# Kernel tuning notes

Hardware: AMD Instinct MI355X
Metric: run time of the kernel (lower is better)

## Reference

```python
import jax, jax.numpy as jnp
import numpy as np

N = 32768   # num nodes
E = 65536   # num edges
H = 64      # hidden_size
EH = 64     # edge_hidden_size
LN_EPS = 1e-5


def setup_inputs() -> dict:
    key = jax.random.key(0)
    ks = jax.random.split(key, 6)
    node_emb = jax.random.normal(ks[0], (N, H), dtype=jnp.float32)
    edge_emb = jax.random.normal(ks[1], (E, EH), dtype=jnp.float32)
    edge_index = jax.random.randint(ks[2], (2, E), 0, N, dtype=jnp.int64)
    # edge_weight_net MLP: edge_hidden -> hidden (relu) -> H*H, xavier-uniform style scales
    W1 = jax.random.normal(ks[3], (EH, H), dtype=jnp.float32) * (2.0 / (EH + H)) ** 0.5
    b1 = jnp.zeros((H,), dtype=jnp.float32)
    W2 = jax.random.normal(ks[4], (H, H * H), dtype=jnp.float32) * (2.0 / (H + H * H)) ** 0.5
    b2 = jnp.zeros((H * H,), dtype=jnp.float32)
    root = jax.random.normal(ks[5], (H, H), dtype=jnp.float32) * (2.0 / (H + H)) ** 0.5
    bias = jnp.zeros((H,), dtype=jnp.float32)
    gamma = jnp.ones((H,), dtype=jnp.float32)
    beta = jnp.zeros((H,), dtype=jnp.float32)
    return {"node_emb": node_emb, "edge_emb": edge_emb, "W1": W1, "b1": b1,
            "W2": W2, "b2": b2, "root": root, "bias": bias,
            "gamma": gamma, "beta": beta, "edge_index": edge_index}


def reference(node_emb, edge_emb, W1, b1, W2, b2, root, bias, gamma, beta, edge_index):
    src, dst = edge_index[0], edge_index[1]
    num_nodes = node_emb.shape[0]
    # edge-conditioned weight: MLP(edge_emb) -> per-edge [H, H] matrix ('full' mode)
    h = jax.nn.relu(edge_emb @ W1 + b1)                 # [E, H]
    W = (h @ W2 + b2).reshape(-1, H, H)                 # [E, H, H]
    # message = x_src @ W_e  (bmm of [1,H] x [H,H] per edge)
    msg = jnp.einsum('eh,ehk->ek', node_emb[src], W)    # [E, H]
    # scatter-add aggregation at destination nodes
    agg = jax.ops.segment_sum(msg, dst, num_segments=num_nodes)          # [N, H]
    deg = jax.ops.segment_sum(jnp.ones_like(dst, dtype=node_emb.dtype), dst,
                              num_segments=num_nodes)                    # [N]
    agg = agg / jnp.maximum(deg, 1.0)[:, None]          # 'mean' aggregation
    # root transform + bias + residual
    out = agg + node_emb @ root + bias + node_emb       # [N, H]
    # LayerNorm over hidden dim
    mu = jnp.mean(out, axis=-1, keepdims=True)
    var = jnp.var(out, axis=-1, keepdims=True)
    out = (out - mu) * jax.lax.rsqrt(var + LN_EPS) * gamma + beta
    return out
```

## Files before the change

### kernel.cpp

```cpp
#include <hip/hip_runtime.h>

#define N_NODES 32768
#define N_EDGES 65536

typedef _Float16 f16;
typedef _Float16 f16x8 __attribute__((ext_vector_type(8)));
typedef float f32x16 __attribute__((ext_vector_type(16)));

#define WS_AGG   0
#define WS_DEG   8388608
#define WS_W2    8519680
#define WS_W1    9060352
#define WS_ROOT  9068544

#define MFMA(a, b, c) __builtin_amdgcn_mfma_f32_32x32x16_f16((a), (b), (c), 0, 0, 0)

__device__ inline f16 u16_as_f16(unsigned short u) {
  union { unsigned short s; f16 h; } v; v.s = u; return v.h;
}
__device__ inline f16x8 splat8(f16 x) {
  f16x8 r;
  #pragma unroll
  for (int u = 0; u < 8; ++u) r[u] = x;
  return r;
}
__device__ inline f16x8 cvt8(float4 p0, float4 p1) {
  f16x8 a;
  a[0] = (f16)p0.x; a[1] = (f16)p0.y; a[2] = (f16)p0.z; a[3] = (f16)p0.w;
  a[4] = (f16)p1.x; a[5] = (f16)p1.y; a[6] = (f16)p1.z; a[7] = (f16)p1.w;
  return a;
}

__global__ __launch_bounds__(256) void k_prep(const float* __restrict__ W1,
                                              const float* __restrict__ W2,
                                              const float* __restrict__ b2,
                                              const float* __restrict__ root,
                                              const int* __restrict__ eidx,
                                              float* __restrict__ deg,
                                              char* __restrict__ w2v2,
                                              char* __restrict__ w1v2,
                                              char* __restrict__ rootIv2) {
  int t = blockIdx.x * 256 + threadIdx.x;
  if (t < 270336) {
    int oct = t >> 9, q = t & 511;
    int col = q >> 3, hl = q & 7;
    int j = oct >> 3, sub = oct & 7;
    int h = (sub >> 1) * 16 + (sub & 1) * 8 + hl;
    float v = 0.f;
    if (j < 64)       v = W2[j * 4096 + h * 64 + col];
    else if (j == 64) v = b2[h * 64 + col];
    *(f16*)(w2v2 + t * 2) = (f16)v;
  } else if (t < 274432) {
    int u = t - 270336;
    int oct = u >> 9, q = u & 511, col = q >> 3, hl = q & 7;
    int i = (oct >> 1) * 16 + (oct & 1) * 8 + hl;
    *(f16*)(w1v2 + u * 2) = (f16)W1[i * 64 + col];
  } else if (t < 278528) {
    int u = t - 274432;
    int oct = u >> 9, q = u & 511, col = q >> 3, hl = q & 7;
    int i = (oct >> 1) * 16 + (oct & 1) * 8 + hl;
    float v = root[i * 64 + col] + (i == col ? 1.f : 0.f);
    *(f16*)(rootIv2 + u * 2) = (f16)v;
  } else if (t < 344064) {
    int e = t - 278528;
    unsafeAtomicAdd(&deg[eidx[N_EDGES + e]], 1.0f);
  }
}

__global__ __launch_bounds__(256, 1) void k_main(const float* __restrict__ node,
                                                 const float* __restrict__ edge,
                                                 const float* __restrict__ b1,
                                                 const int* __restrict__ eidx,
                                                 const char* __restrict__ w2v2,
                                                 const char* __restrict__ w1v2,
                                                 float* __restrict__ agg) {
  __shared__ char ldsH[34816];

  const int tid = threadIdx.x;
  const int lane = tid & 63;
  const int wv = tid >> 6;
  const int ln31 = lane & 31;
  const int half = lane >> 5;
  const int ebase = blockIdx.x * 256;

  const char* w1p = w1v2 + half * 1024 + ln31 * 16;
  #pragma unroll
  for (int t = 0; t < 2; ++t) {
    const int tile = 2 * wv + t;
    const int e = ebase + tile * 32 + ln31;
    const float4* er = (const float4*)edge + (long)e * 16;
    f32x16 c0 = {}, c1 = {};
    #pragma unroll
    for (int kk = 0; kk < 4; ++kk) {
      f16x8 a = cvt8(er[kk * 4 + half * 2], er[kk * 4 + half * 2 + 1]);
      f16x8 bf0 = *(const f16x8*)(w1p + (kk * 2 << 10));
      f16x8 bf1 = *(const f16x8*)(w1p + (kk * 2 << 10) + 512);
      c0 = MFMA(a, bf0, c0);
      c1 = MFMA(a, bf1, c1);
    }
    const float bb0 = b1[ln31], bb1 = b1[32 + ln31];
    char* hb = ldsH + tile * 32 * 136;
    #pragma unroll
    for (int r = 0; r < 16; ++r) {
      const int m = (r & 3) + 8 * (r >> 2) + 4 * half;
      *(f16*)(hb + m * 136 + ln31 * 2)      = (f16)fmaxf(c0[r] + bb0, 0.f);
      *(f16*)(hb + m * 136 + 64 + ln31 * 2) = (f16)fmaxf(c1[r] + bb1, 0.f);
    }
  }

  const int ch = wv & 1;
  const int g  = wv >> 1;

  f16x8 xf[4][4];
  #pragma unroll
  for (int t = 0; t < 4; ++t) {
    const int e = ebase + (g * 4 + t) * 32 + ln31;
    const int s = eidx[e];
    const float4* xr = (const float4*)node + (long)s * 16;
    #pragma unroll
    for (int kk = 0; kk < 4; ++kk)
      xf[t][kk] = cvt8(xr[kk * 4 + half * 2], xr[kk * 4 + half * 2 + 1]);
  }

  const char* wp = w2v2 + half * 1024 + ch * 512 + ln31 * 16;
  f16x8 bufA[8], bufB[8];
  #pragma unroll
  for (int jj = 0; jj < 2; ++jj)
    #pragma unroll
    for (int kk = 0; kk < 4; ++kk)
      bufA[jj * 4 + kk] = *(const f16x8*)(wp + ((jj * 8 + kk * 2) << 10));

  f32x16 acc[4] = {};
  const char* hp[4];
  #pragma unroll
  for (int t = 0; t < 4; ++t) hp[t] = ldsH + (g * 128 + t * 32 + ln31) * 136;

  __syncthreads();

  for (int cp = 0; cp < 16; ++cp) {
    const char* base = wp + (cp << 15);
    uint2 hv[4];
    #pragma unroll
    for (int t = 0; t < 4; ++t) hv[t] = *(const uint2*)(hp[t] + cp * 8);

    #pragma unroll
    for (int jj = 0; jj < 2; ++jj)
      #pragma unroll
      for (int kk = 0; kk < 4; ++kk)
        bufB[jj * 4 + kk] = *(const f16x8*)(base + 16384 + ((jj * 8 + kk * 2) << 10));

    #pragma unroll
    for (int jj = 0; jj < 2; ++jj) {
      f16x8 sp[4];
      #pragma unroll
      for (int t = 0; t < 4; ++t)
        sp[t] = splat8(u16_as_f16((unsigned short)(hv[t].x >> (jj * 16))));
      #pragma unroll
      for (int kk = 0; kk < 4; ++kk)
        #pragma unroll
        for (int t = 0; t < 4; ++t)
          acc[t] = MFMA(xf[t][kk] * sp[t], bufA[jj * 4 + kk], acc[t]);
    }

    #pragma unroll
    for (int jj = 0; jj < 2; ++jj)
      #pragma unroll
      for (int kk = 0; kk < 4; ++kk)
        bufA[jj * 4 + kk] = *(const f16x8*)(base + 32768 + ((jj * 8 + kk * 2) << 10));

    #pragma unroll
    for (int jj = 0; jj < 2; ++jj) {
      f16x8 sp[4];
      #pragma unroll
      for (int t = 0; t < 4; ++t)
        sp[t] = splat8(u16_as_f16((unsigned short)(hv[t].y >> (jj * 16))));
      #pragma unroll
      for (int kk = 0; kk < 4; ++kk)
        #pragma unroll
        for (int t = 0; t < 4; ++t)
          acc[t] = MFMA(xf[t][kk] * sp[t], bufB[jj * 4 + kk], acc[t]);
    }
  }

  #pragma unroll
  for (int kk = 0; kk < 4; ++kk)
    #pragma unroll
    for (int t = 0; t < 4; ++t)
      acc[t] = MFMA(xf[t][kk], bufA[kk], acc[t]);

  #pragma unroll
  for (int t = 0; t < 4; ++t) {
    const int base_e = ebase + (g * 4 + t) * 32;
    #pragma unroll
    for (int r = 0; r < 16; ++r) {
      const int m = (r & 3) + 8 * (r >> 2) + 4 * half;
      const int d = eidx[N_EDGES + base_e + m];
      unsafeAtomicAdd(&agg[(long)d * 64 + ch * 32 + ln31], acc[t][r]);
    }
  }
}

__global__ __launch_bounds__(256) void k_node(const float* __restrict__ node,
                                              const float* __restrict__ agg,
                                              const float* __restrict__ deg,
                                              const char* __restrict__ rootIv2,
                                              const float* __restrict__ bias,
                                              const float* __restrict__ gamma,
                                              const float* __restrict__ beta,
                                              float* __restrict__ out) {
  const int tid = threadIdx.x;
  const int lane = tid & 63;
  const int wv = tid >> 6;
  const int ln31 = lane & 31;
  const int half = lane >> 5;
  const int nb = blockIdx.x * 128 + wv * 32;

  const char* rp = rootIv2 + half * 1024 + ln31 * 16;
  f32x16 c0 = {}, c1 = {};
  const float4* xr = (const float4*)node + (long)(nb + ln31) * 16;
  #pragma unroll
  for (int kk = 0; kk < 4; ++kk) {
    f16x8 a = cvt8(xr[kk * 4 + half * 2], xr[kk * 4 + half * 2 + 1]);
    f16x8 b0 = *(const f16x8*)(rp + (kk * 2 << 10));
    f16x8 b1f = *(const f16x8*)(rp + (kk * 2 << 10) + 512);
    c0 = MFMA(a, b0, c0);
    c1 = MFMA(a, b1f, c1);
  }
  const float bi0 = bias[ln31],  bi1 = bias[32 + ln31];
  const float g0  = gamma[ln31], g1  = gamma[32 + ln31];
  const float be0 = beta[ln31],  be1 = beta[32 + ln31];
  #pragma unroll
  for (int r = 0; r < 16; ++r) {
    const int m = (r & 3) + 8 * (r >> 2) + 4 * half;
    const int n = nb + m;
    const float rd = 1.f / fmaxf(deg[n], 1.f);
    const float pre0 = agg[n * 64 + ln31] * rd + c0[r] + bi0;
    const float pre1 = agg[n * 64 + 32 + ln31] * rd + c1[r] + bi1;
    float s = pre0 + pre1, s2 = pre0 * pre0 + pre1 * pre1;
    #pragma unroll
    for (int mk = 16; mk >= 1; mk >>= 1) {
      s  += __shfl_xor(s, mk, 64);
      s2 += __shfl_xor(s2, mk, 64);
    }
    const float mu  = s * 0.015625f;
    const float var = s2 * 0.015625f - mu * mu;
    const float inv = rsqrtf(var + 1e-5f);
    out[n * 64 + ln31]      = (pre0 - mu) * inv * g0 + be0;
    out[n * 64 + 32 + ln31] = (pre1 - mu) * inv * g1 + be1;
  }
}

extern "C" void kernel_launch(void* const* d_in, const int* in_sizes, int n_in,
                              void* d_out, int out_size, void* d_ws, size_t ws_size,
                              hipStream_t stream) {
  const float* node  = (const float*)d_in[0];
  const float* edgee = (const float*)d_in[1];
  const float* W1    = (const float*)d_in[2];
  const float* b1    = (const float*)d_in[3];
  const float* W2    = (const float*)d_in[4];
  const float* b2    = (const float*)d_in[5];
  const float* root  = (const float*)d_in[6];
  const float* bias  = (const float*)d_in[7];
  const float* gamma = (const float*)d_in[8];
  const float* beta  = (const float*)d_in[9];
  const int*   eidx  = (const int*)d_in[10];
  float* out = (float*)d_out;

  char* ws = (char*)d_ws;
  float* agg     = (float*)(ws + WS_AGG);
  float* deg     = (float*)(ws + WS_DEG);
  char*  w2v2    = ws + WS_W2;
  char*  w1v2    = ws + WS_W1;
  char*  rootIv2 = ws + WS_ROOT;

  hipMemsetAsync(ws, 0, 8519680, stream);

  k_prep<<<1344, 256, 0, stream>>>(W1, W2, b2, root, eidx, deg, w2v2, w1v2, rootIv2);
  k_main<<<256, 256, 0, stream>>>(node, edgee, b1, eidx, w2v2, w1v2, agg);
  k_node<<<256, 256, 0, stream>>>(node, agg, deg, rootIv2, bias, gamma, beta, out);
}
```

Before: 143.4 us.

## Double k_main wavefronts, halve per-wave edge tiles, and vectorize weight prep

k_main now runs 512 threads per block, so each wave handles two edge tiles instead of four. This cuts register pressure and raises the number of resident waves. The main loop is rewritten as a double-buffered chunk load/compute pipeline with s_setprio hints around the MFMA blocks. The b2 bias term is folded in by writing a constant 1.0 into the LDS hidden row. k_prep is also vectorized to read float4 and scatter f16 values, which cuts its thread count. The tradeoff is that each W2 fragment is reused across fewer edges per wave, so W2 traffic from L2 rises.

```diff
diff --git a/kernel.cpp b/kernel.cpp
--- a/kernel.cpp
+++ b/kernel.cpp
@@ -6,6 +6,7 @@
 typedef _Float16 f16;
 typedef _Float16 f16x8 __attribute__((ext_vector_type(8)));
 typedef float f32x16 __attribute__((ext_vector_type(16)));
+typedef unsigned int uint32;
 
 #define WS_AGG   0
 #define WS_DEG   8388608
@@ -41,33 +42,77 @@
                                               char* __restrict__ w1v2,
                                               char* __restrict__ rootIv2) {
   int t = blockIdx.x * 256 + threadIdx.x;
-  if (t < 270336) {
-    int oct = t >> 9, q = t & 511;
-    int col = q >> 3, hl = q & 7;
-    int j = oct >> 3, sub = oct & 7;
-    int h = (sub >> 1) * 16 + (sub & 1) * 8 + hl;
-    float v = 0.f;
-    if (j < 64)       v = W2[j * 4096 + h * 64 + col];
-    else if (j == 64) v = b2[h * 64 + col];
-    *(f16*)(w2v2 + t * 2) = (f16)v;
-  } else if (t < 274432) {
-    int u = t - 270336;
-    int oct = u >> 9, q = u & 511, col = q >> 3, hl = q & 7;
-    int i = (oct >> 1) * 16 + (oct & 1) * 8 + hl;
-    *(f16*)(w1v2 + u * 2) = (f16)W1[i * 64 + col];
-  } else if (t < 278528) {
-    int u = t - 274432;
-    int oct = u >> 9, q = u & 511, col = q >> 3, hl = q & 7;
-    int i = (oct >> 1) * 16 + (oct & 1) * 8 + hl;
-    float v = root[i * 64 + col] + (i == col ? 1.f : 0.f);
-    *(f16*)(rootIv2 + u * 2) = (f16)v;
-  } else if (t < 344064) {
-    int e = t - 278528;
+  if (t < 65536) {
+    int j = t >> 10, rem = t & 1023, h = rem >> 4, c4 = rem & 15;
+    float4 v = *(const float4*)(W2 + j * 4096 + h * 64 + c4 * 4);
+    int oct = j * 8 + (h >> 4) * 2 + ((h >> 3) & 1);
+    char* base = w2v2 + oct * 1024 + (h & 7) * 2;
+    *(f16*)(base + (c4 * 4 + 0) * 16) = (f16)v.x;
+    *(f16*)(base + (c4 * 4 + 1) * 16) = (f16)v.y;
+    *(f16*)(base + (c4 * 4 + 2) * 16) = (f16)v.z;
+    *(f16*)(base + (c4 * 4 + 3) * 16) = (f16)v.w;
+  } else if (t < 66560) {
+    int u = t - 65536, h = u >> 4, c4 = u & 15;
+    float4 v = *(const float4*)(b2 + h * 64 + c4 * 4);
+    int oct = 512 + (h >> 4) * 2 + ((h >> 3) & 1);
+    char* base = w2v2 + oct * 1024 + (h & 7) * 2;
+    *(f16*)(base + (c4 * 4 + 0) * 16) = (f16)v.x;
+    *(f16*)(base + (c4 * 4 + 1) * 16) = (f16)v.y;
+    *(f16*)(base + (c4 * 4 + 2) * 16) = (f16)v.z;
+    *(f16*)(base + (c4 * 4 + 3) * 16) = (f16)v.w;
+  } else if (t < 67584) {
+    int u = t - 66560, h = u >> 4, c4 = u & 15;
+    int oct = 520 + (h >> 4) * 2 + ((h >> 3) & 1);
+    char* base = w2v2 + oct * 1024 + (h & 7) * 2;
+    #pragma unroll
+    for (int q = 0; q < 4; ++q) *(f16*)(base + (c4 * 4 + q) * 16) = (f16)0.f;
+  } else if (t < 68608) {
+    int u = t - 67584, i = u >> 4, c4 = u & 15;
+    float4 v = *(const float4*)(W1 + i * 64 + c4 * 4);
+    int oct = (i >> 4) * 2 + ((i >> 3) & 1);
+    char* base = w1v2 + oct * 1024 + (i & 7) * 2;
+    *(f16*)(base + (c4 * 4 + 0) * 16) = (f16)v.x;
+    *(f16*)(base + (c4 * 4 + 1) * 16) = (f16)v.y;
+    *(f16*)(base + (c4 * 4 + 2) * 16) = (f16)v.z;
+    *(f16*)(base + (c4 * 4 + 3) * 16) = (f16)v.w;
+  } else if (t < 69632) {
+    int u = t - 68608, i = u >> 4, c4 = u & 15;
+    float4 v = *(const float4*)(root + i * 64 + c4 * 4);
+    int oct = (i >> 4) * 2 + ((i >> 3) & 1);
+    char* base = rootIv2 + oct * 1024 + (i & 7) * 2;
+    *(f16*)(base + (c4 * 4 + 0) * 16) = (f16)(v.x + (i == c4 * 4 + 0 ? 1.f : 0.f));
+    *(f16*)(base + (c4 * 4 + 1) * 16) = (f16)(v.y + (i == c4 * 4 + 1 ? 1.f : 0.f));
+    *(f16*)(base + (c4 * 4 + 2) * 16) = (f16)(v.z + (i == c4 * 4 + 2 ? 1.f : 0.f));
+    *(f16*)(base + (c4 * 4 + 3) * 16) = (f16)(v.w + (i == c4 * 4 + 3 ? 1.f : 0.f));
+  } else if (t < 135168) {
+    int e = t - 69632;
     unsafeAtomicAdd(&deg[eidx[N_EDGES + e]], 1.0f);
   }
 }
 
-__global__ __launch_bounds__(256, 1) void k_main(const float* __restrict__ node,
+__device__ inline void chunk_load(f16x8 (&buf)[8], const char* wp, int c) {
+  #pragma unroll
+  for (int jj = 0; jj < 2; ++jj)
+    #pragma unroll
+    for (int kk = 0; kk < 4; ++kk)
+      buf[jj * 4 + kk] = *(const f16x8*)(wp + c * 16384 + ((jj * 8 + kk * 2) << 10));
+}
+
+__device__ inline void chunk_compute(const f16x8 (&buf)[8], uint32 hA, uint32 hB,
+                                     const f16x8 (&xf)[2][4], f32x16 (&acc)[2]) {
+  #pragma unroll
+  for (int jj = 0; jj < 2; ++jj) {
+    const f16x8 spA = splat8(u16_as_f16((unsigned short)(hA >> (jj * 16))));
+    const f16x8 spB = splat8(u16_as_f16((unsigned short)(hB >> (jj * 16))));
+    #pragma unroll
+    for (int kk = 0; kk < 4; ++kk) {
+      acc[0] = MFMA(xf[0][kk] * spA, buf[jj * 4 + kk], acc[0]);
+      acc[1] = MFMA(xf[1][kk] * spB, buf[jj * 4 + kk], acc[1]);
+    }
+  }
+}
+
+__global__ __launch_bounds__(512, 2) void k_main(const float* __restrict__ node,
                                                  const float* __restrict__ edge,
                                                  const float* __restrict__ b1,
                                                  const int* __restrict__ eidx,
@@ -83,11 +128,9 @@
   const int half = lane >> 5;
   const int ebase = blockIdx.x * 256;
 
-  const char* w1p = w1v2 + half * 1024 + ln31 * 16;
-  #pragma unroll
-  for (int t = 0; t < 2; ++t) {
-    const int tile = 2 * wv + t;
-    const int e = ebase + tile * 32 + ln31;
+  {
+    const char* w1p = w1v2 + half * 1024 + ln31 * 16;
+    const int e = ebase + wv * 32 + ln31;
     const float4* er = (const float4*)edge + (long)e * 16;
     f32x16 c0 = {}, c1 = {};
     #pragma unroll
@@ -99,22 +142,24 @@
       c1 = MFMA(a, bf1, c1);
     }
     const float bb0 = b1[ln31], bb1 = b1[32 + ln31];
-    char* hb = ldsH + tile * 32 * 136;
+    char* hb = ldsH + wv * 32 * 136;
     #pragma unroll
     for (int r = 0; r < 16; ++r) {
       const int m = (r & 3) + 8 * (r >> 2) + 4 * half;
       *(f16*)(hb + m * 136 + ln31 * 2)      = (f16)fmaxf(c0[r] + bb0, 0.f);
       *(f16*)(hb + m * 136 + 64 + ln31 * 2) = (f16)fmaxf(c1[r] + bb1, 0.f);
     }
-  }
-
+    if (half == 0)
+      *(uint32*)(hb + ln31 * 136 + 128) = 0x00003C00u;
+  }
+
+  const int g = wv >> 1;
   const int ch = wv & 1;
-  const int g  = wv >> 1;
-
-  f16x8 xf[4][4];
-  #pragma unroll
-  for (int t = 0; t < 4; ++t) {
-    const int e = ebase + (g * 4 + t) * 32 + ln31;
+
+  f16x8 xf[2][4];
+  #pragma unroll
+  for (int t = 0; t < 2; ++t) {
+    const int e = ebase + (2 * g + t) * 32 + ln31;
     const int s = eidx[e];
     const float4* xr = (const float4*)node + (long)s * 16;
     #pragma unroll
@@ -123,74 +168,38 @@
   }
 
   const char* wp = w2v2 + half * 1024 + ch * 512 + ln31 * 16;
-  f16x8 bufA[8], bufB[8];
-  #pragma unroll
-  for (int jj = 0; jj < 2; ++jj)
-    #pragma unroll
-    for (int kk = 0; kk < 4; ++kk)
-      bufA[jj * 4 + kk] = *(const f16x8*)(wp + ((jj * 8 + kk * 2) << 10));
-
-  f32x16 acc[4] = {};
-  const char* hp[4];
-  #pragma unroll
-  for (int t = 0; t < 4; ++t) hp[t] = ldsH + (g * 128 + t * 32 + ln31) * 136;
+  const char* hpA = ldsH + ((2 * g + 0) * 32 + ln31) * 136;
+  const char* hpB = ldsH + ((2 * g + 1) * 32 + ln31) * 136;
+
+  f16x8 b0[8], b1v[8];
+  f32x16 acc[2] = {};
+  chunk_load(b0, wp, 0);
 
   __syncthreads();
 
-  for (int cp = 0; cp < 16; ++cp) {
-    const char* base = wp + (cp << 15);
-    uint2 hv[4];
-    #pragma unroll
-    for (int t = 0; t < 4; ++t) hv[t] = *(const uint2*)(hp[t] + cp * 8);
-
-    #pragma unroll
-    for (int jj = 0; jj < 2; ++jj)
-      #pragma unroll
-      for (int kk = 0; kk < 4; ++kk)
-        bufB[jj * 4 + kk] = *(const f16x8*)(base + 16384 + ((jj * 8 + kk * 2) << 10));
-
-    #pragma unroll
-    for (int jj = 0; jj < 2; ++jj) {
-      f16x8 sp[4];
-      #pragma unroll
-      for (int t = 0; t < 4; ++t)
-        sp[t] = splat8(u16_as_f16((unsigned short)(hv[t].x >> (jj * 16))));
-      #pragma unroll
-      for (int kk = 0; kk < 4; ++kk)
-        #pragma unroll
-        for (int t = 0; t < 4; ++t)
-          acc[t] = MFMA(xf[t][kk] * sp[t], bufA[jj * 4 + kk], acc[t]);
-    }
-
-    #pragma unroll
-    for (int jj = 0; jj < 2; ++jj)
-      #pragma unroll
-      for (int kk = 0; kk < 4; ++kk)
-        bufA[jj * 4 + kk] = *(const f16x8*)(base + 32768 + ((jj * 8 + kk * 2) << 10));
-
-    #pragma unroll
-    for (int jj = 0; jj < 2; ++jj) {
-      f16x8 sp[4];
-      #pragma unroll
-      for (int t = 0; t < 4; ++t)
-        sp[t] = splat8(u16_as_f16((unsigned short)(hv[t].y >> (jj * 16))));
-      #pragma unroll
-      for (int kk = 0; kk < 4; ++kk)
-        #pragma unroll
-        for (int t = 0; t < 4; ++t)
-          acc[t] = MFMA(xf[t][kk] * sp[t], bufB[jj * 4 + kk], acc[t]);
-    }
-  }
-
-  #pragma unroll
-  for (int kk = 0; kk < 4; ++kk)
-    #pragma unroll
-    for (int t = 0; t < 4; ++t)
-      acc[t] = MFMA(xf[t][kk], bufA[kk], acc[t]);
-
-  #pragma unroll
-  for (int t = 0; t < 4; ++t) {
-    const int base_e = ebase + (g * 4 + t) * 32;
+  for (int c = 0; c < 32; c += 2) {
+    chunk_load(b1v, wp, c + 1);
+    const uint32 hA0 = *(const uint32*)(hpA + c * 4);
+    const uint32 hB0 = *(const uint32*)(hpB + c * 4);
+    const uint32 hA1 = *(const uint32*)(hpA + c * 4 + 4);
+    const uint32 hB1 = *(const uint32*)(hpB + c * 4 + 4);
+    __builtin_amdgcn_s_setprio(1);
+    chunk_compute(b0, hA0, hB0, xf, acc);
+    __builtin_amdgcn_s_setprio(0);
+    chunk_load(b0, wp, c + 2);
+    __builtin_amdgcn_s_setprio(1);
+    chunk_compute(b1v, hA1, hB1, xf, acc);
+    __builtin_amdgcn_s_setprio(0);
+  }
+  {
+    const uint32 hA = *(const uint32*)(hpA + 128);
+    const uint32 hB = *(const uint32*)(hpB + 128);
+    chunk_compute(b0, hA, hB, xf, acc);
+  }
+
+  #pragma unroll
+  for (int t = 0; t < 2; ++t) {
+    const int base_e = ebase + (2 * g + t) * 32;
     #pragma unroll
     for (int r = 0; r < 16; ++r) {
       const int m = (r & 3) + 8 * (r >> 2) + 4 * half;
@@ -275,7 +284,7 @@
 
   hipMemsetAsync(ws, 0, 8519680, stream);
 
-  k_prep<<<1344, 256, 0, stream>>>(W1, W2, b2, root, eidx, deg, w2v2, w1v2, rootIv2);
-  k_main<<<256, 256, 0, stream>>>(node, edgee, b1, eidx, w2v2, w1v2, agg);
+  k_prep<<<528, 256, 0, stream>>>(W1, W2, b2, root, eidx, deg, w2v2, w1v2, rootIv2);
+  k_main<<<256, 512, 0, stream>>>(node, edgee, b1, eidx, w2v2, w1v2, agg);
   k_node<<<256, 256, 0, stream>>>(node, agg, deg, rootIv2, bias, gamma, beta, out);
 }
```

Result: no change. 146.2 us (+2.0%).

## Replace float atomic scatter with CSR bucketing of fp16 messages and gather-reduce

Applied to the files above, without the earlier changes.

Builds a destination histogram plus an exclusive scan to get CSR offsets. The main kernel writes each message in fp16 into its destination slot using an atomic cursor, instead of doing float atomics into an agg buffer. The node kernel then sums each node's messages with a per-node loop. This drops the 8 MB agg memset and the per-element float atomics, and halves the message traffic. In exchange it adds a single-block scan kernel, a sync point inside the main kernel, fp16 rounding of messages, and uneven per-node loops in the node kernel. The prep kernel is also rewritten to use vectorized float4 reads.

```diff
diff --git a/kernel.cpp b/kernel.cpp
--- a/kernel.cpp
+++ b/kernel.cpp
@@ -6,12 +6,15 @@
 typedef _Float16 f16;
 typedef _Float16 f16x8 __attribute__((ext_vector_type(8)));
 typedef float f32x16 __attribute__((ext_vector_type(16)));
-
-#define WS_AGG   0
-#define WS_DEG   8388608
-#define WS_W2    8519680
-#define WS_W1    9060352
-#define WS_ROOT  9068544
+typedef unsigned int uint32;
+
+#define WS_HIST  0
+#define WS_OFF   131072
+#define WS_CUR   262144
+#define WS_W2    393216
+#define WS_W1    933888
+#define WS_ROOT  942080
+#define WS_MSG   950272
 
 #define MFMA(a, b, c) __builtin_amdgcn_mfma_f32_32x32x16_f16((a), (b), (c), 0, 0, 0)
 
@@ -36,35 +39,98 @@
                                               const float* __restrict__ b2,
                                               const float* __restrict__ root,
                                               const int* __restrict__ eidx,
-                                              float* __restrict__ deg,
+                                              int* __restrict__ hist,
                                               char* __restrict__ w2v2,
                                               char* __restrict__ w1v2,
                                               char* __restrict__ rootIv2) {
   int t = blockIdx.x * 256 + threadIdx.x;
-  if (t < 270336) {
-    int oct = t >> 9, q = t & 511;
-    int col = q >> 3, hl = q & 7;
-    int j = oct >> 3, sub = oct & 7;
-    int h = (sub >> 1) * 16 + (sub & 1) * 8 + hl;
-    float v = 0.f;
-    if (j < 64)       v = W2[j * 4096 + h * 64 + col];
-    else if (j == 64) v = b2[h * 64 + col];
-    *(f16*)(w2v2 + t * 2) = (f16)v;
-  } else if (t < 274432) {
-    int u = t - 270336;
-    int oct = u >> 9, q = u & 511, col = q >> 3, hl = q & 7;
-    int i = (oct >> 1) * 16 + (oct & 1) * 8 + hl;
-    *(f16*)(w1v2 + u * 2) = (f16)W1[i * 64 + col];
-  } else if (t < 278528) {
-    int u = t - 274432;
-    int oct = u >> 9, q = u & 511, col = q >> 3, hl = q & 7;
-    int i = (oct >> 1) * 16 + (oct & 1) * 8 + hl;
-    float v = root[i * 64 + col] + (i == col ? 1.f : 0.f);
-    *(f16*)(rootIv2 + u * 2) = (f16)v;
-  } else if (t < 344064) {
-    int e = t - 278528;
-    unsafeAtomicAdd(&deg[eidx[N_EDGES + e]], 1.0f);
-  }
+  if (t < 65536) {
+    int j = t >> 10, rem = t & 1023, h = rem >> 4, c4 = rem & 15;
+    float4 v = *(const float4*)(W2 + j * 4096 + h * 64 + c4 * 4);
+    int oct = j * 8 + (h >> 4) * 2 + ((h >> 3) & 1);
+    char* base = w2v2 + oct * 1024 + (h & 7) * 2;
+    *(f16*)(base + (c4 * 4 + 0) * 16) = (f16)v.x;
+    *(f16*)(base + (c4 * 4 + 1) * 16) = (f16)v.y;
+    *(f16*)(base + (c4 * 4 + 2) * 16) = (f16)v.z;
+    *(f16*)(base + (c4 * 4 + 3) * 16) = (f16)v.w;
+  } else if (t < 66560) {
+    int u = t - 65536, h = u >> 4, c4 = u & 15;
+    float4 v = *(const float4*)(b2 + h * 64 + c4 * 4);
+    int oct = 512 + (h >> 4) * 2 + ((h >> 3) & 1);
+    char* base = w2v2 + oct * 1024 + (h & 7) * 2;
+    *(f16*)(base + (c4 * 4 + 0) * 16) = (f16)v.x;
+    *(f16*)(base + (c4 * 4 + 1) * 16) = (f16)v.y;
+    *(f16*)(base + (c4 * 4 + 2) * 16) = (f16)v.z;
+    *(f16*)(base + (c4 * 4 + 3) * 16) = (f16)v.w;
+  } else if (t < 67584) {
+    int u = t - 66560, h = u >> 4, c4 = u & 15;
+    int oct = 520 + (h >> 4) * 2 + ((h >> 3) & 1);
+    char* base = w2v2 + oct * 1024 + (h & 7) * 2;
+    #pragma unroll
+    for (int q = 0; q < 4; ++q) *(f16*)(base + (c4 * 4 + q) * 16) = (f16)0.f;
+  } else if (t < 68608) {
+    int u = t - 67584, i = u >> 4, c4 = u & 15;
+    float4 v = *(const float4*)(W1 + i * 64 + c4 * 4);
+    int oct = (i >> 4) * 2 + ((i >> 3) & 1);
+    char* base = w1v2 + oct * 1024 + (i & 7) * 2;
+    *(f16*)(base + (c4 * 4 + 0) * 16) = (f16)v.x;
+    *(f16*)(base + (c4 * 4 + 1) * 16) = (f16)v.y;
+    *(f16*)(base + (c4 * 4 + 2) * 16) = (f16)v.z;
+    *(f16*)(base + (c4 * 4 + 3) * 16) = (f16)v.w;
+  } else if (t < 69632) {
+    int u = t - 68608, i = u >> 4, c4 = u & 15;
+    float4 v = *(const float4*)(root + i * 64 + c4 * 4);
+    int oct = (i >> 4) * 2 + ((i >> 3) & 1);
+    char* base = rootIv2 + oct * 1024 + (i & 7) * 2;
+    *(f16*)(base + (c4 * 4 + 0) * 16) = (f16)(v.x + (i == c4 * 4 + 0 ? 1.f : 0.f));
+    *(f16*)(base + (c4 * 4 + 1) * 16) = (f16)(v.y + (i == c4 * 4 + 1 ? 1.f : 0.f));
+    *(f16*)(base + (c4 * 4 + 2) * 16) = (f16)(v.z + (i == c4 * 4 + 2 ? 1.f : 0.f));
+    *(f16*)(base + (c4 * 4 + 3) * 16) = (f16)(v.w + (i == c4 * 4 + 3 ? 1.f : 0.f));
+  } else if (t < 135168) {
+    int e = t - 69632;
+    atomicAdd(&hist[eidx[N_EDGES + e]], 1);
+  }
+}
+
+__global__ __launch_bounds__(1024) void k_scan(const int* __restrict__ hist,
+                                               int* __restrict__ off,
+                                               int* __restrict__ cursor) {
+  __shared__ int wsum[16];
+  const int tid = threadIdx.x;
+  const int lane = tid & 63;
+  const int wv = tid >> 6;
+  int v[32];
+  const int base = tid * 32;
+  #pragma unroll
+  for (int i = 0; i < 32; ++i) v[i] = hist[base + i];
+  int run = 0;
+  #pragma unroll
+  for (int i = 0; i < 32; ++i) { int x = v[i]; v[i] = run; run += x; }
+  int inc = run;
+  #pragma unroll
+  for (int d = 1; d < 64; d <<= 1) {
+    int o = __shfl_up(inc, d, 64);
+    if (lane >= d) inc += o;
+  }
+  if (lane == 63) wsum[wv] = inc;
+  __syncthreads();
+  int wexcl = 0;
+  for (int i = 0; i < wv; ++i) wexcl += wsum[i];
+  const int texcl = wexcl + inc - run;
+  #pragma unroll
+  for (int i = 0; i < 32; ++i) {
+    const int val = texcl + v[i];
+    off[base + i] = val;
+    cursor[base + i] = val;
+  }
+}
+
+__device__ inline void chunk_load(f16x8 (&buf)[8], const char* p) {
+  #pragma unroll
+  for (int jj = 0; jj < 2; ++jj)
+    #pragma unroll
+    for (int kk = 0; kk < 4; ++kk)
+      buf[jj * 4 + kk] = *(const f16x8*)(p + ((jj * 8 + kk * 2) << 10));
 }
 
 __global__ __launch_bounds__(256, 1) void k_main(const float* __restrict__ node,
@@ -73,8 +139,10 @@
                                                  const int* __restrict__ eidx,
                                                  const char* __restrict__ w2v2,
                                                  const char* __restrict__ w1v2,
-                                                 float* __restrict__ agg) {
+                                                 int* __restrict__ cursor,
+                                                 f16* __restrict__ msg) {
   __shared__ char ldsH[34816];
+  __shared__ int ldsPos[256];
 
   const int tid = threadIdx.x;
   const int lane = tid & 63;
@@ -124,11 +192,7 @@
 
   const char* wp = w2v2 + half * 1024 + ch * 512 + ln31 * 16;
   f16x8 bufA[8], bufB[8];
-  #pragma unroll
-  for (int jj = 0; jj < 2; ++jj)
-    #pragma unroll
-    for (int kk = 0; kk < 4; ++kk)
-      bufA[jj * 4 + kk] = *(const f16x8*)(wp + ((jj * 8 + kk * 2) << 10));
+  chunk_load(bufA, wp);
 
   f32x16 acc[4] = {};
   const char* hp[4];
@@ -143,11 +207,7 @@
     #pragma unroll
     for (int t = 0; t < 4; ++t) hv[t] = *(const uint2*)(hp[t] + cp * 8);
 
-    #pragma unroll
-    for (int jj = 0; jj < 2; ++jj)
-      #pragma unroll
-      for (int kk = 0; kk < 4; ++kk)
-        bufB[jj * 4 + kk] = *(const f16x8*)(base + 16384 + ((jj * 8 + kk * 2) << 10));
+    chunk_load(bufB, base + 16384);
 
     #pragma unroll
     for (int jj = 0; jj < 2; ++jj) {
@@ -162,11 +222,7 @@
           acc[t] = MFMA(xf[t][kk] * sp[t], bufA[jj * 4 + kk], acc[t]);
     }
 
-    #pragma unroll
-    for (int jj = 0; jj < 2; ++jj)
-      #pragma unroll
-      for (int kk = 0; kk < 4; ++kk)
-        bufA[jj * 4 + kk] = *(const f16x8*)(base + 32768 + ((jj * 8 + kk * 2) << 10));
+    chunk_load(bufA, base + 32768);
 
     #pragma unroll
     for (int jj = 0; jj < 2; ++jj) {
@@ -188,21 +244,37 @@
     for (int t = 0; t < 4; ++t)
       acc[t] = MFMA(xf[t][kk], bufA[kk], acc[t]);
 
+  if (ch == 0) {
+    #pragma unroll
+    for (int t = 0; t < 4; ++t) {
+      const int base_e = ebase + (g * 4 + t) * 32;
+      #pragma unroll
+      for (int r = 0; r < 16; ++r) {
+        const int m = (r & 3) + 8 * (r >> 2) + 4 * half;
+        if (ln31 == 0) {
+          const int d = eidx[N_EDGES + base_e + m];
+          ldsPos[(g * 4 + t) * 32 + m] = atomicAdd(&cursor[d], 1);
+        }
+      }
+    }
+  }
+  __syncthreads();
+
   #pragma unroll
   for (int t = 0; t < 4; ++t) {
-    const int base_e = ebase + (g * 4 + t) * 32;
     #pragma unroll
     for (int r = 0; r < 16; ++r) {
       const int m = (r & 3) + 8 * (r >> 2) + 4 * half;
-      const int d = eidx[N_EDGES + base_e + m];
-      unsafeAtomicAdd(&agg[(long)d * 64 + ch * 32 + ln31], acc[t][r]);
+      const int pos = ldsPos[(g * 4 + t) * 32 + m];
+      msg[(long)pos * 64 + ch * 32 + ln31] = (f16)acc[t][r];
     }
   }
 }
 
 __global__ __launch_bounds__(256) void k_node(const float* __restrict__ node,
-                                              const float* __restrict__ agg,
-                                              const float* __restrict__ deg,
+                                              const f16* __restrict__ msg,
+                                              const int* __restrict__ hist,
+                                              const int* __restrict__ off,
                                               const char* __restrict__ rootIv2,
                                               const float* __restrict__ bias,
                                               const float* __restrict__ gamma,
@@ -233,9 +305,17 @@
   for (int r = 0; r < 16; ++r) {
     const int m = (r & 3) + 8 * (r >> 2) + 4 * half;
     const int n = nb + m;
-    const float rd = 1.f / fmaxf(deg[n], 1.f);
-    const float pre0 = agg[n * 64 + ln31] * rd + c0[r] + bi0;
-    const float pre1 = agg[n * 64 + 32 + ln31] * rd + c1[r] + bi1;
+    const int cnt = hist[n];
+    const int start = off[n];
+    float s0 = 0.f, s1 = 0.f;
+    for (int k = 0; k < cnt; ++k) {
+      const f16* mr = msg + (long)(start + k) * 64;
+      s0 += (float)mr[ln31];
+      s1 += (float)mr[32 + ln31];
+    }
+    const float rd = 1.f / fmaxf((float)cnt, 1.f);
+    const float pre0 = s0 * rd + c0[r] + bi0;
+    const float pre1 = s1 * rd + c1[r] + bi1;
     float s = pre0 + pre1, s2 = pre0 * pre0 + pre1 * pre1;
     #pragma unroll
     for (int mk = 16; mk >= 1; mk >>= 1) {
@@ -267,15 +347,18 @@
   float* out = (float*)d_out;
 
   char* ws = (char*)d_ws;
-  float* agg     = (float*)(ws + WS_AGG);
-  float* deg     = (float*)(ws + WS_DEG);
+  int*   hist    = (int*)(ws + WS_HIST);
+  int*   off     = (int*)(ws + WS_OFF);
+  int*   cursor  = (int*)(ws + WS_CUR);
   char*  w2v2    = ws + WS_W2;
   char*  w1v2    = ws + WS_W1;
   char*  rootIv2 = ws + WS_ROOT;
-
-  hipMemsetAsync(ws, 0, 8519680, stream);
-
-  k_prep<<<1344, 256, 0, stream>>>(W1, W2, b2, root, eidx, deg, w2v2, w1v2, rootIv2);
-  k_main<<<256, 256, 0, stream>>>(node, edgee, b1, eidx, w2v2, w1v2, agg);
-  k_node<<<256, 256, 0, stream>>>(node, agg, deg, rootIv2, bias, gamma, beta, out);
-}
+  f16*   msg     = (f16*)(ws + WS_MSG);
+
+  hipMemsetAsync(hist, 0, 131072, stream);
+
+  k_prep<<<528, 256, 0, stream>>>(W1, W2, b2, root, eidx, hist, w2v2, w1v2, rootIv2);
+  k_scan<<<1, 1024, 0, stream>>>(hist, off, cursor);
+  k_main<<<256, 256, 0, stream>>>(node, edgee, b1, eidx, w2v2, w1v2, cursor, msg);
+  k_node<<<256, 256, 0, stream>>>(node, msg, hist, off, rootIv2, bias, gamma, beta, out);
+}
```

Measured after the change: 177.3 us. 1.24x slower.
